# Kernel tuning notes

Measured on AMD Instinct MI355X. Metric: run time of the kernel, lower is better.

Reference implementation:

```python
import jax, jax.numpy as jnp
import numpy as np

EPS = 1e-8
TAU = 1.0


def _spatial_adjacency(segments, n_seg):
    # segments: (B, H, W) int. Counts 4-neighbour pixel adjacencies between segments;
    # diagonal counts pixels per segment (self loops kept).
    B, H, W = segments.shape
    b = jnp.arange(B)[:, None]
    adj = jnp.zeros((B, n_seg, n_seg), jnp.float32)
    flat = segments.reshape(B, -1)
    adj = adj.at[b, flat, flat].add(1.0)  # self loops = segment sizes
    s1 = segments[:, :, :-1].reshape(B, -1)
    s2 = segments[:, :, 1:].reshape(B, -1)
    adj = adj.at[b, s1, s2].add(1.0).at[b, s2, s1].add(1.0)
    v1 = segments[:, :-1, :].reshape(B, -1)
    v2 = segments[:, 1:, :].reshape(B, -1)
    adj = adj.at[b, v1, v2].add(1.0).at[b, v2, v1].add(1.0)
    return adj


def _proximity_adjacency(segments, n_seg):
    adj = _spatial_adjacency(segments, n_seg)
    # zero connections of node 0 except its diagonal
    adj = adj.at[:, 1:, 0].set(0.0).at[:, 0, 1:].set(0.0)
    size_node = jnp.diagonal(adj, axis1=-2, axis2=-1)
    new_diag = adj.sum(axis=2) - size_node + 1.0
    idx = jnp.arange(n_seg)
    adj = adj.at[:, idx, idx].set(new_diag)
    # normalize_adjacency(binarize=True, normalize=False)
    return (adj > 0).astype(jnp.float32)


def setup_inputs() -> dict:
    key = jax.random.key(0)
    k1, k2, k3 = jax.random.split(key, 3)
    B, N, D, R = 8, 2048, 384, 64
    H = W = 256
    x = jax.random.normal(k1, (B, N, D), jnp.float32)
    segments = jax.random.randint(k2, (B, H, W), 0, N, jnp.int64)
    prototypes = jax.random.normal(k3, (1, R, D), jnp.float32)
    return {"x": x, "segments": segments, "prototypes": prototypes}


def reference(x, segments, prototypes):
    B, N, D = x.shape
    prox_adj = _proximity_adjacency(segments, N)  # (B, N, N) binary

    # node-presence mask (B, N)
    b = jnp.arange(B)[:, None]
    flat = segments.reshape(B, -1)
    mask = jnp.zeros((B, N), jnp.float32).at[b, flat].max(1.0)

    # cosine prototype clustering (Q = V = K = Identity)
    protos = prototypes[0]  # (R, D)
    qn = x / jnp.maximum(jnp.linalg.norm(x, axis=-1, keepdims=True), EPS)
    kn = protos / jnp.maximum(jnp.linalg.norm(protos, axis=-1, keepdims=True), EPS)
    Csim = (jnp.einsum('bnd,rd->bnr', qn, kn) + 1.0) * 0.5
    S = Csim / Csim.sum(axis=-1, keepdims=True)  # soft assignment (B, N, R)

    # cluster alignment loss (DEC-style sharpened-target KL, masked over present nodes)
    P = S ** 2 / (S.sum(axis=1, keepdims=True) + EPS)
    P = P / (P.sum(axis=-1, keepdims=True) + EPS)
    kl = (P * (jnp.log(P + EPS) - jnp.log(S + EPS))).sum(axis=-1)  # (B, N)
    loss = (kl * mask).sum() / (mask.sum() + EPS)

    # affinity adjacency from assignments
    C = jax.nn.softmax(S * TAU, axis=-1)  # (B, N, R)
    cn = jnp.linalg.norm(C, axis=-1)  # (B, N)
    proto_adj = jnp.einsum('bnr,bmr->bnm', C, C) / (cn[:, :, None] * cn[:, None, :] + EPS)
    adj = prox_adj * proto_adj
    # normalize_adjacency(normalize=True): row normalization
    adj = adj / (adj.sum(axis=-1, keepdims=True) + EPS)

    out = jnp.einsum('bnm,bmd->bnd', adj, x)  # adj @ values
    return out, segments, loss, C
```

## Files before the change

kernel.cpp:

```cpp
#include <hip/hip_runtime.h>
#include <hip/hip_bf16.h>

#define NB 8
#define NN 2048
#define ND 384
#define NR 64
#define OUT_ELEMS (NB*NN*ND)
#define SEG_ELEMS (NB*256*256)
#define NBLK_LOSS (NB*NN/4)

typedef float  f32x4  __attribute__((ext_vector_type(4)));
typedef short  bf16x8 __attribute__((ext_vector_type(8)));

__device__ inline float wsum(float v){
  #pragma unroll
  for(int o=32;o;o>>=1) v += __shfl_xor(v,o,64);
  return v;
}
__device__ inline float wmax(float v){
  #pragma unroll
  for(int o=32;o;o>>=1) v = fmaxf(v,__shfl_xor(v,o,64));
  return v;
}
__device__ inline unsigned short f2bf(float f){
  unsigned u = __float_as_uint(f);
  return (unsigned short)((u + 0x8000u) >> 16);
}

__device__ __forceinline__ void gl2lds16(const unsigned short* g, unsigned short* s){
  __builtin_amdgcn_global_load_lds(
      (const __attribute__((address_space(1))) unsigned int*)g,
      (__attribute__((address_space(3))) unsigned int*)s,
      16, 0, 0);
}

__global__ void k_proto(const float* __restrict__ protos, float* __restrict__ kn){
  int r = blockIdx.x, l = threadIdx.x;
  float v[6]; float ss = 0.f;
  #pragma unroll
  for(int i=0;i<6;i++){ v[i] = protos[r*ND + l*6 + i]; ss += v[i]*v[i]; }
  ss = wsum(ss);
  float inv = 1.f / fmaxf(sqrtf(ss), 1e-8f);
  #pragma unroll
  for(int i=0;i<6;i++) kn[r*ND + l*6 + i] = v[i]*inv;
}

__global__ __launch_bounds__(1024) void k_seg(const int* __restrict__ seg,
                                              float* __restrict__ mask,
                                              unsigned* __restrict__ prox){
  __shared__ unsigned lm[64*64];
  int tid = threadIdx.x;
  int b  = blockIdx.x & 7;
  int rg = blockIdx.x >> 3;
  int base = rg << 6;
  for(int i=tid; i<64*64; i+=1024) lm[i] = 0u;
  __syncthreads();
  const int* sb = seg + b*65536;

#define PAIR(S, S2) { \
    if((S) != (S2) && (S) != 0 && (S2) != 0){ \
      if(((S )>>6)==rg) atomicOr(&lm[(((S )&63)<<6) + ((S2)>>5)], 1u<<((S2)&31)); \
      if(((S2)>>6)==rg) atomicOr(&lm[(((S2)&63)<<6) + ((S )>>5)], 1u<<((S )&31)); \
    } }

  #pragma unroll 1
  for(int it=0; it<16; ++it){
    int g = it*1024 + tid;
    int p = g*4;
    int i = g >> 6;
    int j = (g & 63)*4;
    int4 a = *(const int4*)(sb + p);
    if((a.x>>6)==rg) mask[(b<<11) + a.x] = 1.f;
    if((a.y>>6)==rg) mask[(b<<11) + a.y] = 1.f;
    if((a.z>>6)==rg) mask[(b<<11) + a.z] = 1.f;
    if((a.w>>6)==rg) mask[(b<<11) + a.w] = 1.f;
    PAIR(a.x, a.y); PAIR(a.y, a.z); PAIR(a.z, a.w);
    if(j < 252){
      int n = sb[p + 4];
      PAIR(a.w, n);
    }
    if(i < 255){
      int4 v = *(const int4*)(sb + p + 256);
      PAIR(a.x, v.x); PAIR(a.y, v.y); PAIR(a.z, v.z); PAIR(a.w, v.w);
    }
  }
#undef PAIR
  __syncthreads();
  unsigned* dst = prox + ((size_t)(b<<11) + base)*64;
  *(uint4*)(dst + tid*4) = *(const uint4*)&lm[tid*4];
}

__global__ __launch_bounds__(256) void k_csim(const float* __restrict__ x,
                                              const float* __restrict__ kn,
                                              float* __restrict__ Sout,
                                              unsigned short* __restrict__ xTbf,
                                              float* __restrict__ part){
  __shared__ float xT[32*68];
  __shared__ float kT[32*68];
  __shared__ float xinvS[64];
  __shared__ float csh[16*64];
  int t = threadIdx.x;
  int m0 = blockIdx.x * 64;
  float acc[4][4] = {};
  int mload = t>>2, koff = (t&3)*8;
  int mb = (t>>4)*4, rb = (t&15)*4;
  float ssq = 0.f;
  for(int c=0;c<12;c++){
    int k0 = c*32;
    __syncthreads();
    const float4* xg = (const float4*)(x + (size_t)(m0+mload)*ND + k0 + koff);
    float4 a = xg[0], bq = xg[1];
    ssq += a.x*a.x + a.y*a.y + a.z*a.z + a.w*a.w
         + bq.x*bq.x + bq.y*bq.y + bq.z*bq.z + bq.w*bq.w;
    xT[(koff+0)*68+mload]=a.x;  xT[(koff+1)*68+mload]=a.y;  xT[(koff+2)*68+mload]=a.z;  xT[(koff+3)*68+mload]=a.w;
    xT[(koff+4)*68+mload]=bq.x; xT[(koff+5)*68+mload]=bq.y; xT[(koff+6)*68+mload]=bq.z; xT[(koff+7)*68+mload]=bq.w;
    const float4* kg = (const float4*)(kn + mload*ND + k0 + koff);
    float4 ka = kg[0], kb = kg[1];
    kT[(koff+0)*68+mload]=ka.x; kT[(koff+1)*68+mload]=ka.y; kT[(koff+2)*68+mload]=ka.z; kT[(koff+3)*68+mload]=ka.w;
    kT[(koff+4)*68+mload]=kb.x; kT[(koff+5)*68+mload]=kb.y; kT[(koff+6)*68+mload]=kb.z; kT[(koff+7)*68+mload]=kb.w;
    __syncthreads();
    {
      int k2 = t>>3, mo = (t&7)*8;
      const float* src = &xT[k2*68 + mo];
      float4 aa = *(const float4*)src;
      float4 bb = *(const float4*)(src+4);
      uint4 o;
      o.x = (unsigned)f2bf(aa.x) | ((unsigned)f2bf(aa.y)<<16);
      o.y = (unsigned)f2bf(aa.z) | ((unsigned)f2bf(aa.w)<<16);
      o.z = (unsigned)f2bf(bb.x) | ((unsigned)f2bf(bb.y)<<16);
      o.w = (unsigned)f2bf(bb.z) | ((unsigned)f2bf(bb.w)<<16);
      int bb2 = m0 >> 11, ml = m0 & 2047;
      *(uint4*)(xTbf + ((size_t)(bb2*ND + k0 + k2))*NN + ml + mo) = o;
    }
    for(int k=0;k<32;k++){
      float xv[4], kv[4];
      *(float4*)xv = *(const float4*)&xT[k*68+mb];
      *(float4*)kv = *(const float4*)&kT[k*68+rb];
      #pragma unroll
      for(int mi=0;mi<4;mi++)
        #pragma unroll
        for(int ri=0;ri<4;ri++) acc[mi][ri] += xv[mi]*kv[ri];
    }
  }
  ssq += __shfl_xor(ssq,1,64);
  ssq += __shfl_xor(ssq,2,64);
  if((t&3)==0) xinvS[mload] = 1.f / fmaxf(sqrtf(ssq), 1e-8f);
  __syncthreads();
  float sv[4][4];
  #pragma unroll
  for(int mi=0;mi<4;mi++){
    float xin = xinvS[mb+mi];
    float rsum = 0.f;
    #pragma unroll
    for(int ri=0;ri<4;ri++){
      float vv = (acc[mi][ri]*xin + 1.f)*0.5f;
      sv[mi][ri] = vv; rsum += vv;
    }
    rsum += __shfl_xor(rsum,1,64);
    rsum += __shfl_xor(rsum,2,64);
    rsum += __shfl_xor(rsum,4,64);
    rsum += __shfl_xor(rsum,8,64);
    float inv = 1.f/rsum;
    #pragma unroll
    for(int ri=0;ri<4;ri++) sv[mi][ri] *= inv;
    *(float4*)&Sout[(size_t)(m0+mb+mi)*NR + rb] = *(const float4*)sv[mi];
  }
  {
    float4 pc;
    pc.x = sv[0][0]+sv[1][0]+sv[2][0]+sv[3][0];
    pc.y = sv[0][1]+sv[1][1]+sv[2][1]+sv[3][1];
    pc.z = sv[0][2]+sv[1][2]+sv[2][2]+sv[3][2];
    pc.w = sv[0][3]+sv[1][3]+sv[2][3]+sv[3][3];
    *(float4*)&csh[(t>>4)*64 + rb] = pc;
  }
  __syncthreads();
  if(t < 64){
    float a = 0.f;
    #pragma unroll
    for(int g=0;g<16;g++) a += csh[g*64 + t];
    part[(size_t)blockIdx.x*64 + t] = a;
  }
}

__global__ void k_lossfc(float* Smat, const float* __restrict__ part,
                         const float* __restrict__ mask,
                         float* __restrict__ klp, float* __restrict__ mp,
                         unsigned short* __restrict__ Kbf){
  __shared__ float shk[4], shm[4];
  int w = threadIdx.x>>6, l = threadIdx.x&63;
  int node = blockIdx.x*4 + w;
  int b = node >> 11;
  float s = Smat[(size_t)node*NR + l];
  float csm = 0.f;
  #pragma unroll
  for(int c=0;c<32;c++) csm += part[(size_t)((b<<5)+c)*64 + l];
  float p = s*s/(csm + 1e-8f);
  float ps = wsum(p);
  float P = p/(ps + 1e-8f);
  float term = P*(logf(P + 1e-8f) - logf(s + 1e-8f));
  float kl = wsum(term);
  if(l==0){ float mv = mask[node]; shk[w] = kl*mv; shm[w] = mv; }
  float mx = wmax(s);
  float e = expf(s - mx);
  float Z = wsum(e);
  float c = e / Z;
  float cn2 = wsum(c*c);
  Smat[(size_t)node*NR + l] = c;
  Kbf[(size_t)node*NR + l] = f2bf(c * rsqrtf(cn2));
  __syncthreads();
  if(threadIdx.x==0){
    klp[blockIdx.x] = shk[0]+shk[1]+shk[2]+shk[3];
    mp [blockIdx.x] = shm[0]+shm[1]+shm[2]+shm[3];
  }
}

__global__ __launch_bounds__(256, 3) void k_qkpv(const unsigned short* __restrict__ Kbf,
                                                 const unsigned* __restrict__ prox,
                                                 const unsigned short* __restrict__ xTbf,
                                                 float* __restrict__ out){
  __shared__ unsigned short Al[64*64];
  __shared__ unsigned short Bl[128*64];
  int tid = threadIdx.x;
  int w = tid>>6, l = tid&63, q = l>>4, li = l&15;
  int b  = blockIdx.x & 7;
  int mt = (blockIdx.x>>3) & 31;
  int ct = blockIdx.x >> 8;
  int m0 = mt*64;
  int d0 = ct*128;
  const unsigned short* Kb   = Kbf  + (size_t)b*NN*NR;
  const unsigned short* xTb  = xTbf + (size_t)b*ND*NN;

  int wr = w & 1, wc = w >> 1;

  int lrow8 = l>>3;
  int sgel  = ((l&7) ^ lrow8) * 8;
  const unsigned short* gsrc[4];
  unsigned short* ldst[4];
  #pragma unroll
  for(int j=0;j<4;j++){
    int id = w*4 + j;
    ldst[j] = Bl + id*512;
    gsrc[j] = xTb + (size_t)(d0 + id*8 + lrow8)*NN + sgel;
  }

  const unsigned short* bmp = Kb + (size_t)(m0 + w*16 + li)*NR + q*8;
  bf16x8 bm0 = *(const bf16x8*)bmp;
  bf16x8 bm1 = *(const bf16x8*)(bmp + 32);
  const unsigned* prxp = prox + ((size_t)(b*NN + m0 + w*16 + li))*64;
  int diagidx = w*16 + li;

  f32x4 acc[2][4];
  #pragma unroll
  for(int nc=0;nc<2;nc++)
    #pragma unroll
    for(int t=0;t<4;t++) acc[nc][t] = (f32x4)(0.f);
  f32x4 rs[2] = {(f32x4)(0.f),(f32x4)(0.f)};
  bf16x8 ones;
  #pragma unroll
  for(int i=0;i<8;i++) ones[i] = (short)0x3F80;

  int r7 = li & 7;
  for(int k0=0; k0<NN; k0+=64){
    __syncthreads();
    bf16x8 ka0[4], ka1[4];
    #pragma unroll
    for(int f=0;f<4;f++){
      const unsigned short* p = Kb + (size_t)(k0 + f*16 + li)*NR + q*8;
      ka0[f] = *(const bf16x8*)p;
      ka1[f] = *(const bf16x8*)(p + 32);
    }
    #pragma unroll
    for(int j=0;j<4;j++) gl2lds16(gsrc[j] + k0, ldst[j]);
    uint2 mw = *(const uint2*)(prxp + (k0>>5));

    f32x4 pacc[4] = {(f32x4)(0.f),(f32x4)(0.f),(f32x4)(0.f),(f32x4)(0.f)};
    #pragma unroll
    for(int f=0;f<4;f++){
      pacc[f] = __builtin_amdgcn_mfma_f32_16x16x32_bf16(ka0[f], bm0, pacc[f], 0,0,0);
      pacc[f] = __builtin_amdgcn_mfma_f32_16x16x32_bf16(ka1[f], bm1, pacc[f], 0,0,0);
    }
    bool dg = (k0 == m0);
    #pragma unroll
    for(int f=0;f<4;f++){
      unsigned wd = (f<2) ? mw.x : mw.y;
      float v[4];
      #pragma unroll
      for(int r=0;r<4;r++){
        int bit = ((f&1)*16) + q*4 + r;
        bool on = (wd >> bit) & 1u;
        if(dg && (f*16 + q*4 + r) == diagidx) on = true;
        v[r] = on ? pacc[f][r] : 0.f;
      }
      uint2 pk;
      pk.x = (unsigned)f2bf(v[0]) | ((unsigned)f2bf(v[1])<<16);
      pk.y = (unsigned)f2bf(v[2]) | ((unsigned)f2bf(v[3])<<16);
      int eoff = (w*16 + li)*64 + (((f*2 + (q>>1)) ^ r7) * 8) + (q&1)*4;
      *(uint2*)&Al[eoff] = pk;
    }
    __syncthreads();

    #pragma unroll
    for(int s=0;s<2;s++){
      int ps = ((s*4 + q) ^ r7) * 8;
      bf16x8 a0 = *(const bf16x8*)&Al[(wr*32 +      li)*64 + ps];
      bf16x8 a1 = *(const bf16x8*)&Al[(wr*32 + 16 + li)*64 + ps];
      bf16x8 bv[4];
      #pragma unroll
      for(int t=0;t<4;t++)
        bv[t] = *(const bf16x8*)&Bl[(wc*64 + t*16 + li)*64 + ps];
      #pragma unroll
      for(int t=0;t<4;t++){
        acc[0][t] = __builtin_amdgcn_mfma_f32_16x16x32_bf16(a0, bv[t], acc[0][t], 0,0,0);
        acc[1][t] = __builtin_amdgcn_mfma_f32_16x16x32_bf16(a1, bv[t], acc[1][t], 0,0,0);
      }
      rs[0] = __builtin_amdgcn_mfma_f32_16x16x32_bf16(a0, ones, rs[0], 0,0,0);
      rs[1] = __builtin_amdgcn_mfma_f32_16x16x32_bf16(a1, ones, rs[1], 0,0,0);
    }
  }

  #pragma unroll
  for(int nc=0;nc<2;nc++)
    #pragma unroll
    for(int r=0;r<4;r++){
      int row = m0 + wr*32 + nc*16 + q*4 + r;
      float inv = 1.f/(rs[nc][r] + 1e-8f);
      float* orow = out + ((size_t)(b*NN + row))*ND + d0 + wc*64;
      #pragma unroll
      for(int t=0;t<4;t++)
        orow[t*16 + li] = acc[nc][t][r] * inv;
    }
}

__global__ void k_segout(const int* __restrict__ seg, float* __restrict__ o,
                         const float* __restrict__ klp, const float* __restrict__ mp,
                         float* __restrict__ outLoss){
  int tid = threadIdx.x;
  int i = blockIdx.x*256 + tid;
  o[i] = (float)seg[i];
  if(blockIdx.x==0){
    __shared__ float sa[4], sm[4];
    float a=0.f, m=0.f;
    for(int k=tid; k<NBLK_LOSS; k+=256){ a += klp[k]; m += mp[k]; }
    a = wsum(a); m = wsum(m);
    if((tid&63)==0){ sa[tid>>6]=a; sm[tid>>6]=m; }
    __syncthreads();
    if(tid==0)
      outLoss[0] = (sa[0]+sa[1]+sa[2]+sa[3])/((sm[0]+sm[1]+sm[2]+sm[3])+1e-8f);
  }
}

extern "C" void kernel_launch(void* const* d_in, const int* in_sizes, int n_in,
                              void* d_out, int out_size, void* d_ws, size_t ws_size,
                              hipStream_t stream) {
  const float* x      = (const float*)d_in[0];
  const int*   seg    = (const int*)d_in[1];
  const float* protos = (const float*)d_in[2];

  float* out     = (float*)d_out;
  float* outSeg  = out + OUT_ELEMS;
  float* outLoss = outSeg + SEG_ELEMS;
  float* outC    = outLoss + 1;

  unsigned short* xTbf = (unsigned short*)d_ws;
  unsigned short* Kbf  = xTbf + (size_t)NB*ND*NN;
  unsigned short* Pbf  = Kbf + (size_t)NB*NN*NR;
  float* kn      = (float*)(Pbf + (size_t)NB*NN*NN);
  float* maskp   = kn + NR*ND;
  unsigned* prox = (unsigned*)(maskp + NB*NN);
  float* part    = (float*)(prox + (size_t)NB*NN*64);
  float* klp     = part + NB*32*64;
  float* mp      = klp + NBLK_LOSS;

  hipMemsetAsync(maskp, 0, (size_t)NB*NN*4, stream);

  k_proto <<<dim3(NR),           dim3(64),   0, stream>>>(protos, kn);
  k_seg   <<<dim3(256),          dim3(1024), 0, stream>>>(seg, maskp, prox);
  k_csim  <<<dim3(NB*NN/64),     dim3(256),  0, stream>>>(x, kn, outC, xTbf, part);
  k_lossfc<<<dim3(NBLK_LOSS),    dim3(256),  0, stream>>>(outC, part, maskp, klp, mp, Kbf);
  k_qkpv  <<<dim3(768),          dim3(256),  0, stream>>>(Kbf, prox, xTbf, out);
  k_segout<<<dim3(SEG_ELEMS/256),dim3(256),  0, stream>>>(seg, outSeg, klp, mp, outLoss);
}
```

Baseline: 250.3 us.

## Compute proto affinity only on proximity neighbours via sparse neighbor list

Result: slower. 269.2 us (+7.6%).

```diff
diff --git a/kernel.cpp b/kernel.cpp
--- a/kernel.cpp
+++ b/kernel.cpp
@@ -8,6 +8,7 @@
 #define OUT_ELEMS (NB*NN*ND)
 #define SEG_ELEMS (NB*256*256)
 #define NBLK_LOSS (NB*NN/4)
+#define NBCAP 384
 
 typedef float  f32x4  __attribute__((ext_vector_type(4)));
 typedef short  bf16x8 __attribute__((ext_vector_type(8)));
@@ -25,6 +26,9 @@
 __device__ inline unsigned short f2bf(float f){
   unsigned u = __float_as_uint(f);
   return (unsigned short)((u + 0x8000u) >> 16);
+}
+__device__ inline float bf2f(short s){
+  return __uint_as_float(((unsigned)(unsigned short)s) << 16);
 }
 
 __device__ __forceinline__ void gl2lds16(const unsigned short* g, unsigned short* s){
@@ -214,12 +218,63 @@
   }
 }
 
-__global__ __launch_bounds__(256, 3) void k_qkpv(const unsigned short* __restrict__ Kbf,
-                                                 const unsigned* __restrict__ prox,
-                                                 const unsigned short* __restrict__ xTbf,
-                                                 float* __restrict__ out){
+__global__ __launch_bounds__(256) void k_nbr(const unsigned short* __restrict__ Kbf,
+                                             const unsigned* __restrict__ prox,
+                                             unsigned* __restrict__ nbr,
+                                             unsigned short* __restrict__ off){
+  int w = threadIdx.x>>6, L = threadIdx.x&63;
+  int n = blockIdx.x*4 + w;
+  int node = n & (NN-1);
+  const unsigned short* KbB = Kbf + ((size_t)(n >> 11))*NN*NR;
+
+  unsigned word = prox[(size_t)n*64 + L];
+  if(L == (node>>5)) word |= 1u << (node&31);
+  int pc = __popc(word);
+  int pre = pc;
+  #pragma unroll
+  for(int o=1;o<64;o<<=1){
+    int v = __shfl_up(pre, o, 64);
+    if(L >= o) pre += v;
+  }
+  int base = pre - pc;
+  if((L&1)==0) off[(size_t)n*33 + (L>>1)] = (unsigned short)base;
+  if(L==63)    off[(size_t)n*33 + 32]     = (unsigned short)pre;
+
+  const bf16x8* cnp = (const bf16x8*)(Kbf + (size_t)n*NR);
+  float cnf[64];
+  #pragma unroll
+  for(int s=0;s<8;s++){
+    bf16x8 cv = cnp[s];
+    #pragma unroll
+    for(int e=0;e<8;e++) cnf[s*8+e] = bf2f(cv[e]);
+  }
+
+  unsigned* nb = nbr + (size_t)n*NBCAP;
+  int idx = base;
+  while(word){
+    int bit = __ffs(word) - 1;
+    word &= word - 1;
+    int m = (L<<5) + bit;
+    const bf16x8* cmp = (const bf16x8*)(KbB + (size_t)m*NR);
+    float acc = 0.f;
+    #pragma unroll
+    for(int s=0;s<8;s++){
+      bf16x8 cv = cmp[s];
+      #pragma unroll
+      for(int e=0;e<8;e++) acc += cnf[s*8+e]*bf2f(cv[e]);
+    }
+    if(idx < NBCAP) nb[idx] = ((unsigned)m<<16) | (unsigned)f2bf(acc);
+    idx++;
+  }
+}
+
+__global__ __launch_bounds__(256, 3) void k_pv(const unsigned* __restrict__ nbr,
+                                               const unsigned short* __restrict__ off,
+                                               const unsigned short* __restrict__ xTbf,
+                                               float* __restrict__ out){
   __shared__ unsigned short Al[64*64];
   __shared__ unsigned short Bl[128*64];
+  __shared__ unsigned short offL[64*33];
   int tid = threadIdx.x;
   int w = tid>>6, l = tid&63, q = l>>4, li = l&15;
   int b  = blockIdx.x & 7;
@@ -227,8 +282,7 @@
   int ct = blockIdx.x >> 8;
   int m0 = mt*64;
   int d0 = ct*128;
-  const unsigned short* Kb   = Kbf  + (size_t)b*NN*NR;
-  const unsigned short* xTb  = xTbf + (size_t)b*ND*NN;
+  const unsigned short* xTb = xTbf + (size_t)b*ND*NN;
 
   int wr = w & 1, wc = w >> 1;
 
@@ -243,11 +297,11 @@
     gsrc[j] = xTb + (size_t)(d0 + id*8 + lrow8)*NN + sgel;
   }
 
-  const unsigned short* bmp = Kb + (size_t)(m0 + w*16 + li)*NR + q*8;
-  bf16x8 bm0 = *(const bf16x8*)bmp;
-  bf16x8 bm1 = *(const bf16x8*)(bmp + 32);
-  const unsigned* prxp = prox + ((size_t)(b*NN + m0 + w*16 + li))*64;
-  int diagidx = w*16 + li;
+  int srow = tid>>2, g = tid&3;
+  int r7s  = srow & 7;
+  const unsigned* ebase = nbr + (size_t)(b*NN + m0 + srow)*NBCAP;
+  for(int j=g; j<33; j+=4)
+    offL[srow*33 + j] = off[(size_t)(b*NN + m0 + srow)*33 + j];
 
   f32x4 acc[2][4];
   #pragma unroll
@@ -261,41 +315,26 @@
 
   int r7 = li & 7;
   for(int k0=0; k0<NN; k0+=64){
-    __syncthreads();
-    bf16x8 ka0[4], ka1[4];
-    #pragma unroll
-    for(int f=0;f<4;f++){
-      const unsigned short* p = Kb + (size_t)(k0 + f*16 + li)*NR + q*8;
-      ka0[f] = *(const bf16x8*)p;
-      ka1[f] = *(const bf16x8*)(p + 32);
-    }
+    int t = k0 >> 6;
+    __syncthreads();
+    {
+      uint4 z = {0,0,0,0};
+      *(uint4*)&Al[tid*16]     = z;
+      *(uint4*)&Al[tid*16 + 8] = z;
+    }
+    __syncthreads();
     #pragma unroll
     for(int j=0;j<4;j++) gl2lds16(gsrc[j] + k0, ldst[j]);
-    uint2 mw = *(const uint2*)(prxp + (k0>>5));
-
-    f32x4 pacc[4] = {(f32x4)(0.f),(f32x4)(0.f),(f32x4)(0.f),(f32x4)(0.f)};
-    #pragma unroll
-    for(int f=0;f<4;f++){
-      pacc[f] = __builtin_amdgcn_mfma_f32_16x16x32_bf16(ka0[f], bm0, pacc[f], 0,0,0);
-      pacc[f] = __builtin_amdgcn_mfma_f32_16x16x32_bf16(ka1[f], bm1, pacc[f], 0,0,0);
-    }
-    bool dg = (k0 == m0);
-    #pragma unroll
-    for(int f=0;f<4;f++){
-      unsigned wd = (f<2) ? mw.x : mw.y;
-      float v[4];
-      #pragma unroll
-      for(int r=0;r<4;r++){
-        int bit = ((f&1)*16) + q*4 + r;
-        bool on = (wd >> bit) & 1u;
-        if(dg && (f*16 + q*4 + r) == diagidx) on = true;
-        v[r] = on ? pacc[f][r] : 0.f;
+    {
+      int s0 = offL[srow*33 + t];
+      int s1 = offL[srow*33 + t + 1];
+      if(s1 > NBCAP) s1 = NBCAP;
+      for(int i=s0+g; i<s1; i+=4){
+        unsigned e = ebase[i];
+        int col = (int)(e >> 16) - k0;
+        int phys = (((col>>3) ^ r7s) << 3) | (col & 7);
+        Al[srow*64 + phys] = (unsigned short)(e & 0xffffu);
       }
-      uint2 pk;
-      pk.x = (unsigned)f2bf(v[0]) | ((unsigned)f2bf(v[1])<<16);
-      pk.y = (unsigned)f2bf(v[2]) | ((unsigned)f2bf(v[3])<<16);
-      int eoff = (w*16 + li)*64 + (((f*2 + (q>>1)) ^ r7) * 8) + (q&1)*4;
-      *(uint2*)&Al[eoff] = pk;
     }
     __syncthreads();
 
@@ -306,12 +345,12 @@
       bf16x8 a1 = *(const bf16x8*)&Al[(wr*32 + 16 + li)*64 + ps];
       bf16x8 bv[4];
       #pragma unroll
-      for(int t=0;t<4;t++)
-        bv[t] = *(const bf16x8*)&Bl[(wc*64 + t*16 + li)*64 + ps];
+      for(int t2=0;t2<4;t2++)
+        bv[t2] = *(const bf16x8*)&Bl[(wc*64 + t2*16 + li)*64 + ps];
       #pragma unroll
-      for(int t=0;t<4;t++){
-        acc[0][t] = __builtin_amdgcn_mfma_f32_16x16x32_bf16(a0, bv[t], acc[0][t], 0,0,0);
-        acc[1][t] = __builtin_amdgcn_mfma_f32_16x16x32_bf16(a1, bv[t], acc[1][t], 0,0,0);
+      for(int t2=0;t2<4;t2++){
+        acc[0][t2] = __builtin_amdgcn_mfma_f32_16x16x32_bf16(a0, bv[t2], acc[0][t2], 0,0,0);
+        acc[1][t2] = __builtin_amdgcn_mfma_f32_16x16x32_bf16(a1, bv[t2], acc[1][t2], 0,0,0);
       }
       rs[0] = __builtin_amdgcn_mfma_f32_16x16x32_bf16(a0, ones, rs[0], 0,0,0);
       rs[1] = __builtin_amdgcn_mfma_f32_16x16x32_bf16(a1, ones, rs[1], 0,0,0);
@@ -326,8 +365,8 @@
       float inv = 1.f/(rs[nc][r] + 1e-8f);
       float* orow = out + ((size_t)(b*NN + row))*ND + d0 + wc*64;
       #pragma unroll
-      for(int t=0;t<4;t++)
-        orow[t*16 + li] = acc[nc][t][r] * inv;
+      for(int t2=0;t2<4;t2++)
+        orow[t2*16 + li] = acc[nc][t2][r] * inv;
     }
 }
 
@@ -364,6 +403,8 @@
   unsigned short* xTbf = (unsigned short*)d_ws;
   unsigned short* Kbf  = xTbf + (size_t)NB*ND*NN;
   unsigned short* Pbf  = Kbf + (size_t)NB*NN*NR;
+  unsigned*       nbr  = (unsigned*)Pbf;
+  unsigned short* off  = (unsigned short*)(nbr + (size_t)NB*NN*NBCAP);
   float* kn      = (float*)(Pbf + (size_t)NB*NN*NN);
   float* maskp   = kn + NR*ND;
   unsigned* prox = (unsigned*)(maskp + NB*NN);
@@ -377,6 +418,7 @@
   k_seg   <<<dim3(256),          dim3(1024), 0, stream>>>(seg, maskp, prox);
   k_csim  <<<dim3(NB*NN/64),     dim3(256),  0, stream>>>(x, kn, outC, xTbf, part);
   k_lossfc<<<dim3(NBLK_LOSS),    dim3(256),  0, stream>>>(outC, part, maskp, klp, mp, Kbf);
-  k_qkpv  <<<dim3(768),          dim3(256),  0, stream>>>(Kbf, prox, xTbf, out);
+  k_nbr   <<<dim3(NB*NN/4),      dim3(256),  0, stream>>>(Kbf, prox, nbr, off);
+  k_pv    <<<dim3(768),          dim3(256),  0, stream>>>(nbr, off, xTbf, out);
   k_segout<<<dim3(SEG_ELEMS/256),dim3(256),  0, stream>>>(seg, outSeg, klp, mp, outLoss);
 }
```
